# Performance work log

Hardware: AMD Instinct MI355X
Metric: run time of the kernel (lower is better)

The kernel has to match this reference:

```python
import jax, jax.numpy as jnp
import numpy as np


def setup_inputs() -> dict:
    key = jax.random.key(0)
    k1, k2, k3, k4 = jax.random.split(key, 4)
    B, T, N, D = 16, 4, 1601, 1280  # batch, max_num_tiles, tokens/tile, embed_dim
    x = jax.random.normal(k1, (B, T, N, D), dtype=jnp.float32)
    # (h_tiles, w_tiles) per sample, each in [1, 2] so h*w <= max_num_tiles=4
    aspect_ratio = jax.random.randint(k2, (B, 2), 1, 3, dtype=jnp.int64)
    embedding = jax.random.normal(k3, (T, T, 1, D), dtype=jnp.float32) / np.sqrt(D)
    gate = jnp.zeros((1,), dtype=jnp.float32) + 0.1  # nonzero so output depends on embedding
    return {"x": x, "aspect_ratio": aspect_ratio, "embedding": embedding, "gate": gate}


def reference(x, aspect_ratio, embedding, gate):
    # x: (B, T, N, D); embedding: (T, T, 1, D); aspect_ratio: (B, 2) ints
    B, T, N, D = x.shape
    t = jnp.arange(T)[None, :]                    # (1, T) flattened tile index
    h = aspect_ratio[:, 0:1]                      # (B, 1)
    w = aspect_ratio[:, 1:2]                      # (B, 1)
    valid = t < h * w                             # (B, T) tile is non-padded
    row = jnp.where(valid, t // w, 0)             # (B, T)
    col = jnp.where(valid, t % w, 0)              # (B, T)
    pe = embedding[row, col]                      # (B, T, 1, D) gathered pos embeds
    pe = jnp.where(valid[:, :, None, None], pe, jnp.zeros((), x.dtype))
    return x + pe * jnp.tanh(gate)                # broadcast over N tokens
```

## Files before the change

kernel.cpp:

```cpp
#include <hip/hip_runtime.h>
#include <math.h>

#define Bsz 16
#define Tsz 4
#define Nsz 1601
#define Dsz 1280
#define D4  (Dsz / 4)
#define ROWS_PER_BLK 50

typedef float f32x4 __attribute__((ext_vector_type(4)));

__device__ __forceinline__ void load_hw(const int* __restrict__ ar, int b, int& h, int& w) {
    int v0 = ar[2 * b];
    int v1 = ar[2 * b + 1];
    if (v1 != 0) {
        h = v0; w = v1;
    } else {
        h = ar[4 * b];
        w = ar[4 * b + 2];
    }
}

__global__ void build_pe_kernel(const f32x4* __restrict__ emb,
                                const int* __restrict__ ar,
                                const float* __restrict__ gate,
                                f32x4* __restrict__ pe) {
    int bt = blockIdx.x;
    int b = bt >> 2;
    int t = bt & 3;
    int h, w;
    load_hw(ar, b, h, w);
    float tg = tanhf(gate[0]);
    bool valid = t < h * w;
    int d4 = threadIdx.x;
    f32x4 v = (f32x4)(0.f);
    if (valid) {
        int row = t / w;
        int col = t % w;
        v = emb[(row * Tsz + col) * D4 + d4] * tg;
    }
    pe[bt * D4 + d4] = v;
}

__global__ void add_pe_kernel(const f32x4* __restrict__ x,
                              const f32x4* __restrict__ pe,
                              f32x4* __restrict__ out) {
    int bt = blockIdx.y;
    int r0 = blockIdx.x * ROWS_PER_BLK;
    int nrows = min(ROWS_PER_BLK, Nsz - r0);
    f32x4 pv = pe[bt * D4 + threadIdx.x];
    long base = ((long)bt * Nsz + r0) * D4 + threadIdx.x;

    int g = 0;
    for (; g + 1 < nrows; g += 2) {
        f32x4 a = __builtin_nontemporal_load(&x[base + (long)g * D4]);
        f32x4 c = __builtin_nontemporal_load(&x[base + (long)(g + 1) * D4]);
        a += pv;
        c += pv;
        __builtin_nontemporal_store(a, &out[base + (long)g * D4]);
        __builtin_nontemporal_store(c, &out[base + (long)(g + 1) * D4]);
    }
    if (g < nrows) {
        f32x4 a = __builtin_nontemporal_load(&x[base + (long)g * D4]);
        a += pv;
        __builtin_nontemporal_store(a, &out[base + (long)g * D4]);
    }
}

extern "C" void kernel_launch(void* const* d_in, const int* in_sizes, int n_in,
                              void* d_out, int out_size, void* d_ws, size_t ws_size,
                              hipStream_t stream) {
    const f32x4* x    = (const f32x4*)d_in[0];
    const int*   ar   = (const int*)d_in[1];
    const f32x4* emb  = (const f32x4*)d_in[2];
    const float* gate = (const float*)d_in[3];
    f32x4* out = (f32x4*)d_out;

    f32x4* pe = (f32x4*)d_ws;
    build_pe_kernel<<<dim3(Bsz * Tsz), D4, 0, stream>>>(emb, ar, gate, pe);
    int chunks = (Nsz + ROWS_PER_BLK - 1) / ROWS_PER_BLK;
    add_pe_kernel<<<dim3(chunks, Bsz * Tsz), D4, 0, stream>>>(x, pe, out);
}
```

Before: 221.2 us.

## Fuse PE build into add kernel and use grid-stride rows

Removes the separate build_pe kernel launch and its workspace buffer. Each block now computes its positional embedding row inline from the embedding table, aspect ratio and gate. Rows within each (b,t) slice are now split across 24 blocks with a grid-stride loop, giving 64 blocks per slice from 24 instead of 33. This saves one launch and one dependency, at the cost of fewer blocks in flight and redundant embedding and tanh work in every block.

```diff
diff --git a/kernel.cpp b/kernel.cpp
--- a/kernel.cpp
+++ b/kernel.cpp
@@ -6,7 +6,7 @@
 #define Nsz 1601
 #define Dsz 1280
 #define D4  (Dsz / 4)
-#define ROWS_PER_BLK 50
+#define GRIDX 24
 
 typedef float f32x4 __attribute__((ext_vector_type(4)));
 
@@ -21,49 +21,40 @@
     }
 }
 
-__global__ void build_pe_kernel(const f32x4* __restrict__ emb,
-                                const int* __restrict__ ar,
-                                const float* __restrict__ gate,
-                                f32x4* __restrict__ pe) {
-    int bt = blockIdx.x;
+__global__ void add_pe_kernel(const f32x4* __restrict__ x,
+                              const f32x4* __restrict__ emb,
+                              const int* __restrict__ ar,
+                              const float* __restrict__ gate,
+                              f32x4* __restrict__ out) {
+    int bt = blockIdx.y;
     int b = bt >> 2;
     int t = bt & 3;
     int h, w;
     load_hw(ar, b, h, w);
     float tg = tanhf(gate[0]);
-    bool valid = t < h * w;
-    int d4 = threadIdx.x;
-    f32x4 v = (f32x4)(0.f);
-    if (valid) {
+    f32x4 pv = (f32x4)(0.f);
+    if (t < h * w) {
         int row = t / w;
         int col = t % w;
-        v = emb[(row * Tsz + col) * D4 + d4] * tg;
+        pv = emb[(row * Tsz + col) * D4 + threadIdx.x] * tg;
     }
-    pe[bt * D4 + d4] = v;
-}
 
-__global__ void add_pe_kernel(const f32x4* __restrict__ x,
-                              const f32x4* __restrict__ pe,
-                              f32x4* __restrict__ out) {
-    int bt = blockIdx.y;
-    int r0 = blockIdx.x * ROWS_PER_BLK;
-    int nrows = min(ROWS_PER_BLK, Nsz - r0);
-    f32x4 pv = pe[bt * D4 + threadIdx.x];
-    long base = ((long)bt * Nsz + r0) * D4 + threadIdx.x;
+    const long stride = (long)GRIDX * D4;
+    long off = (long)bt * Nsz * D4 + (long)blockIdx.x * D4 + threadIdx.x;
+    const long end = ((long)bt + 1) * Nsz * D4;
 
-    int g = 0;
-    for (; g + 1 < nrows; g += 2) {
-        f32x4 a = __builtin_nontemporal_load(&x[base + (long)g * D4]);
-        f32x4 c = __builtin_nontemporal_load(&x[base + (long)(g + 1) * D4]);
+    for (; off + stride < end; off += 2 * stride) {
+        f32x4 a = __builtin_nontemporal_load(&x[off]);
+        f32x4 c = __builtin_nontemporal_load(&x[off + stride]);
         a += pv;
         c += pv;
-        __builtin_nontemporal_store(a, &out[base + (long)g * D4]);
-        __builtin_nontemporal_store(c, &out[base + (long)(g + 1) * D4]);
+        __builtin_nontemporal_store(a, &out[off]);
+        __builtin_nontemporal_store(c, &out[off + stride]);
     }
-    if (g < nrows) {
-        f32x4 a = __builtin_nontemporal_load(&x[base + (long)g * D4]);
+    if (off < end) {
+        f32x4 a = __builtin_nontemporal_load(&x[off]);
         a += pv;
-        __builtin_nontemporal_store(a, &out[base + (long)g * D4]);
+        __builtin_nontemporal_store(a, &out[off]);
     }
 }
 
@@ -76,8 +67,5 @@
     const float* gate = (const float*)d_in[3];
     f32x4* out = (f32x4*)d_out;
 
-    f32x4* pe = (f32x4*)d_ws;
-    build_pe_kernel<<<dim3(Bsz * Tsz), D4, 0, stream>>>(emb, ar, gate, pe);
-    int chunks = (Nsz + ROWS_PER_BLK - 1) / ROWS_PER_BLK;
-    add_pe_kernel<<<dim3(chunks, Bsz * Tsz), D4, 0, stream>>>(x, pe, out);
+    add_pe_kernel<<<dim3(GRIDX, Bsz * Tsz), D4, 0, stream>>>(x, emb, ar, gate, out);
 }
```

New measurement: 209.9 us. 1.05x faster.
